# Kernel tuning notes

Measured on AMD Instinct MI355X. Metric: run time of the kernel, lower is better.

Reference implementation:

```python
import jax, jax.numpy as jnp
import numpy as np

N_SRC, N_TGT, N_EDGES = 100000, 50000, 1000000
S_IN, T_IN, S_OUT, T_OUT = 128, 128, 64, 64
NEG_SLOPE = 0.2


def setup_inputs() -> dict:
    key = jax.random.key(0)
    ks = jax.random.split(key, 7)
    return {
        "x_source": jax.random.normal(ks[0], (N_SRC, S_IN), jnp.float32),
        "x_target": jax.random.normal(ks[1], (N_TGT, T_IN), jnp.float32),
        "w_s": jax.random.normal(ks[2], (S_IN, T_OUT), jnp.float32) * 0.1,
        "w_t": jax.random.normal(ks[3], (T_IN, S_OUT), jnp.float32) * 0.1,
        "att_weight": jax.random.normal(ks[4], (T_OUT + S_OUT,), jnp.float32) * 0.1,
        "nbhd_values": jnp.ones((N_EDGES,), jnp.float32),
        "rows": jax.random.randint(ks[5], (N_EDGES,), 0, N_TGT, jnp.int32),  # target idx i
        "cols": jax.random.randint(ks[6], (N_EDGES,), 0, N_SRC, jnp.int32),  # source idx j
    }


def reference(x_source, x_target, w_s, w_t, att_weight, nbhd_values, rows, cols):
    n_src, n_tgt = x_source.shape[0], x_target.shape[0]
    t_out = w_s.shape[1]  # dim of s_message
    s_out = w_t.shape[1]  # dim of t_message

    s_msg = x_source @ w_s  # [n_src, t_out]
    t_msg = x_target @ w_t  # [n_tgt, s_out]

    # e_{ij} = LeakyReLU([s_msg_j || t_msg_i] . a); a = [a_s (t_out) || a_t (s_out)]
    a_s, a_t = att_weight[:t_out], att_weight[t_out:]
    # f uses permuted attention vector: [a[s_out:] || a[:s_out]] on [t_msg_j || s_msg_i]
    b_t, b_s = att_weight[s_out:], att_weight[:s_out]

    es = s_msg @ a_s  # [n_src]
    et = t_msg @ a_t  # [n_tgt]
    ft = t_msg @ b_t  # [n_tgt]
    fs = s_msg @ b_s  # [n_src]

    # s->t attention: rows are target cells (row-normalize over target rows)
    e = jax.nn.leaky_relu(es[cols] + et[rows], NEG_SLOPE)  # [E]
    e_den = jax.ops.segment_sum(e, rows, num_segments=n_tgt)
    att_st = e / e_den[rows]

    # t->s attention: transposed indices; rows are source cells
    f = jax.nn.leaky_relu(ft[rows] + fs[cols], NEG_SLOPE)  # [E]
    f_den = jax.ops.segment_sum(f, cols, num_segments=n_src)
    att_ts = f / f_den[cols]

    # Hadamard with neighborhood values, then sparse-dense aggregation
    w_st = att_st * nbhd_values  # [E]
    w_ts = att_ts * nbhd_values  # [E]

    message_on_target = jax.ops.segment_sum(w_st[:, None] * s_msg[cols], rows, num_segments=n_tgt)  # [n_tgt, t_out]
    message_on_source = jax.ops.segment_sum(w_ts[:, None] * t_msg[rows], cols, num_segments=n_src)  # [n_src, s_out]

    # update_func is None -> identity
    return message_on_source, message_on_target
```

## Files before the change

kernel.cpp:

```cpp
#include <hip/hip_runtime.h>

#define N_SRC   100000
#define N_TGT   50000
#define N_EDGES 1000000
#define NEG     0.2
#define NXCD    8
#define TPART   (N_TGT / NXCD)
#define SPART   (N_SRC / NXCD)

#define GBLK_S  1563
#define GBLK_T  782
#define GBLK    (GBLK_S + GBLK_T)
#define NHIST   640


#define XS2 65
__global__ __launch_bounds__(256) void fused_gemm_hist(
    const float* __restrict__ x_source, const float* __restrict__ x_target,
    const float* __restrict__ w_s, const float* __restrict__ w_t,
    const float* __restrict__ att,
    float* __restrict__ s_msg, float* __restrict__ t_msg,
    double* __restrict__ es_d, double* __restrict__ et_d,
    const int* __restrict__ rows, const int* __restrict__ cols,
    int* __restrict__ cnt_r, int* __restrict__ cnt_c,
    unsigned* __restrict__ packT, unsigned* __restrict__ packC)
{
    __shared__ float xs[64 * XS2];
    __shared__ double eds[4][64];
    const int tid = threadIdx.x;

    if (blockIdx.x < NHIST) {
        const int S = NHIST * 256;
        int i = blockIdx.x * 256 + tid;
        for (; i + 3 * S < N_EDGES; i += 4 * S) {
            const unsigned r0 = rows[i],         c0_ = cols[i];
            const unsigned r1 = rows[i + S],     c1_ = cols[i + S];
            const unsigned r2 = rows[i + 2 * S], c2_ = cols[i + 2 * S];
            const unsigned r3 = rows[i + 3 * S], c3_ = cols[i + 3 * S];
            const unsigned kr0 = atomicAdd(&cnt_r[r0], 1);
            const unsigned kc0 = atomicAdd(&cnt_c[c0_], 1);
            const unsigned kr1 = atomicAdd(&cnt_r[r1], 1);
            const unsigned kc1 = atomicAdd(&cnt_c[c1_], 1);
            const unsigned kr2 = atomicAdd(&cnt_r[r2], 1);
            const unsigned kc2 = atomicAdd(&cnt_c[c2_], 1);
            const unsigned kr3 = atomicAdd(&cnt_r[r3], 1);
            const unsigned kc3 = atomicAdd(&cnt_c[c3_], 1);
            packT[i]         = r0 | (kr0 << 16); packC[i]         = c0_ | (kc0 << 17);
            packT[i + S]     = r1 | (kr1 << 16); packC[i + S]     = c1_ | (kc1 << 17);
            packT[i + 2 * S] = r2 | (kr2 << 16); packC[i + 2 * S] = c2_ | (kc2 << 17);
            packT[i + 3 * S] = r3 | (kr3 << 16); packC[i + 3 * S] = c3_ | (kc3 << 17);
        }
        for (; i < N_EDGES; i += S) {
            const unsigned r = rows[i], c = cols[i];
            packT[i] = r | ((unsigned)atomicAdd(&cnt_r[r], 1) << 16);
            packC[i] = c | ((unsigned)atomicAdd(&cnt_c[c], 1) << 17);
        }
        return;
    }

    const int gi = blockIdx.x - NHIST;

    const float* x; const float* w; int att_off, nrows, bblk;
    float* msg; double* evec;
    if (gi < GBLK_S) { x = x_source; w = w_s; att_off = 0;  nrows = N_SRC;
                       msg = s_msg;  evec = es_d; bblk = gi; }
    else             { x = x_target; w = w_t; att_off = 64; nrows = N_TGT;
                       msg = t_msg;  evec = et_d; bblk = gi - GBLK_S; }

    const int lane = tid & 63;
    const int part = tid >> 6;
    const int c0   = __builtin_amdgcn_readfirstlane(part << 4);
    const int row0 = bblk * 64;
    const int row  = row0 + lane;
    const bool act = row < nrows;

    float acc[16];
    #pragma unroll
    for (int c = 0; c < 16; ++c) acc[c] = 0.f;

    const int xbase = lane * XS2;

    #pragma unroll
    for (int it = 0; it < 4; ++it) {
        const int fid = tid + it * 256;
        const int r = fid >> 4, q = fid & 15;
        if (row0 + r < nrows) {
            const float4 v = *(const float4*)(x + (size_t)(row0 + r) * 128 + 4 * q);
            float* d = &xs[r * XS2 + 4 * q];
            d[0] = v.x; d[1] = v.y; d[2] = v.z; d[3] = v.w;
        }
    }
    __syncthreads();

    float4 pre[4];
    #pragma unroll
    for (int it = 0; it < 4; ++it) {
        const int fid = tid + it * 256;
        const int r = fid >> 4, q = fid & 15;
        pre[it] = (row0 + r < nrows)
            ? *(const float4*)(x + (size_t)(row0 + r) * 128 + 64 + 4 * q)
            : make_float4(0.f, 0.f, 0.f, 0.f);
    }

    for (int kc = 0; kc < 64; kc += 16) {
        #pragma unroll
        for (int kk = 0; kk < 16; ++kk) {
            const float xk = xs[xbase + kc + kk];
            const float* wr = w + (size_t)(kc + kk) * 64 + c0;
            #pragma unroll
            for (int c = 0; c < 16; ++c)
                acc[c] = fmaf(xk, wr[c], acc[c]);
        }
    }
    __syncthreads();

    #pragma unroll
    for (int it = 0; it < 4; ++it) {
        const int fid = tid + it * 256;
        const int r = fid >> 4, q = fid & 15;
        float* d = &xs[r * XS2 + 4 * q];
        d[0] = pre[it].x; d[1] = pre[it].y; d[2] = pre[it].z; d[3] = pre[it].w;
    }
    __syncthreads();

    for (int kc = 0; kc < 64; kc += 16) {
        #pragma unroll
        for (int kk = 0; kk < 16; ++kk) {
            const float xk = xs[xbase + kc + kk];
            const float* wr = w + (size_t)(64 + kc + kk) * 64 + c0;
            #pragma unroll
            for (int c = 0; c < 16; ++c)
                acc[c] = fmaf(xk, wr[c], acc[c]);
        }
    }

    double e = 0.0;
    #pragma unroll
    for (int c = 0; c < 16; ++c)
        e += (double)acc[c] * (double)att[att_off + c0 + c];
    eds[part][lane] = e;
    __syncthreads();
    if (part == 0 && act)
        evec[row] = eds[0][lane] + eds[1][lane] + eds[2][lane] + eds[3][lane];

    if (act) {
        float* mo = msg + (size_t)row * 64 + c0;
        #pragma unroll
        for (int q = 0; q < 4; ++q)
            *(float4*)(mo + 4 * q) = *(float4*)(acc + 4 * q);
    }
}

__global__ __launch_bounds__(1024) void scan_two(
    const int* __restrict__ cnt_r, const int* __restrict__ cnt_c,
    int* __restrict__ ptr_r, int* __restrict__ ptr_c)
{
    const int n    = blockIdx.x ? N_SRC : N_TGT;
    const int* cnt = blockIdx.x ? cnt_c : cnt_r;
    int* ptr       = blockIdx.x ? ptr_c : ptr_r;
    const int tid  = threadIdx.x;
    const int lane = tid & 63, wid = tid >> 6;

    __shared__ int wsum[16];
    __shared__ int s_carry;
    if (tid == 0) s_carry = 0;
    __syncthreads();

    for (int base = 0; base < n; base += 4096) {
        const int idx = base + tid * 4;
        int4 v = make_int4(0, 0, 0, 0);
        if (idx + 3 < n) {
            v = *(const int4*)(cnt + idx);
        } else if (idx < n) {
            v.x = cnt[idx];
            if (idx + 1 < n) v.y = cnt[idx + 1];
            if (idx + 2 < n) v.z = cnt[idx + 2];
        }
        const int s = v.x + v.y + v.z + v.w;

        int p = s;
        #pragma unroll
        for (int d = 1; d < 64; d <<= 1) {
            int t = __shfl_up(p, d);
            if (lane >= d) p += t;
        }
        if (lane == 63) wsum[wid] = p;
        __syncthreads();
        if (tid == 0) {
            int a = 0;
            #pragma unroll
            for (int i = 0; i < 16; ++i) { int t = wsum[i]; wsum[i] = a; a += t; }
        }
        __syncthreads();

        int run = s_carry + wsum[wid] + (p - s);
        if (idx     < n) ptr[idx]     = run; run += v.x;
        if (idx + 1 < n) ptr[idx + 1] = run; run += v.y;
        if (idx + 2 < n) ptr[idx + 2] = run; run += v.z;
        if (idx + 3 < n) ptr[idx + 3] = run; run += v.w;

        __syncthreads();
        if (tid == 1023) s_carry = run;
        __syncthreads();
    }
    if (tid == 0) ptr[n] = s_carry;
}

__global__ __launch_bounds__(256) void scatter_part(
    const unsigned* __restrict__ packT, const unsigned* __restrict__ packC,
    const float* __restrict__ nbhd,
    const int* __restrict__ ptr_r, const int* __restrict__ ptr_c,
    unsigned long long* __restrict__ srtT, unsigned long long* __restrict__ srtS)
{
    const int xcd  = blockIdx.x & (NXCD - 1);
    const int ibx  = blockIdx.x >> 3;
    const int step = (gridDim.x >> 3) * blockDim.x;
    const unsigned lo_r = xcd * TPART, lo_c = xcd * SPART;

    for (int i = ibx * blockDim.x + threadIdx.x; i < N_EDGES; i += step) {
        const unsigned pT = packT[i], pC = packC[i];
        const unsigned r = pT & 0xFFFFu,  kr = pT >> 16;
        const unsigned c = pC & 0x1FFFFu, kc = pC >> 17;
        const bool mr = (r - lo_r) < TPART;
        const bool mc = (c - lo_c) < SPART;
        if (!(mr | mc)) continue;
        const unsigned long long nb =
            (unsigned long long)(unsigned)__float_as_int(nbhd[i]) << 32;
        if (mr) srtT[ptr_r[r] + kr] = nb | c;
        if (mc) srtS[ptr_c[c] + kc] = nb | r;
    }
}

__global__ __launch_bounds__(256) void gather_both(
    const int2* __restrict__ srtT, const int* __restrict__ ptr_r,
    const float* __restrict__ s_msg, float* __restrict__ msg_tgt,
    const int2* __restrict__ srtS, const int* __restrict__ ptr_c,
    const float* __restrict__ t_msg, float* __restrict__ msg_src,
    const double* __restrict__ es_d, const double* __restrict__ et_d)
{
    const int gw   = (blockIdx.x * blockDim.x + threadIdx.x) >> 6;
    const int lane = threadIdx.x & 63;

    const int2* srt; const int* ptr; const float* min_; float* out;
    const double* other_d; double base; int row;
    if (gw < N_TGT) {
        srt = srtT; ptr = ptr_r; min_ = s_msg; out = msg_tgt;
        other_d = es_d; row = gw; base = et_d[row];
    } else {
        row = gw - N_TGT;
        if (row >= N_SRC) return;
        srt = srtS; ptr = ptr_c; min_ = t_msg; out = msg_src;
        other_d = et_d; base = es_d[row];
    }

    const int b = ptr[row], e = ptr[row + 1];
    double den = 0.0;
    float a0 = 0.f, a1 = 0.f, a2 = 0.f, a3 = 0.f;

    for (int j0 = b; j0 < e; j0 += 64) {
        const int m = e - j0;
        int oidx = 0; double v = 0.0; float wf = 0.f;
        if (lane < m) {
            const int2 pay = srt[j0 + lane];
            oidx = pay.x;
            const float nb = __int_as_float(pay.y);
            const double sv = base + other_d[oidx];
            v = (sv >= 0.0) ? sv : NEG * sv;
            wf = (float)(v * (double)nb);
        }
        den += v;

        const int cnt = m < 64 ? m : 64;
        int j = 0;
        for (; j + 7 < cnt; j += 8) {
            const int   c0_ = __shfl(oidx, j);     const float w0 = __shfl(wf, j);
            const int   c1_ = __shfl(oidx, j + 1); const float w1 = __shfl(wf, j + 1);
            const int   c2_ = __shfl(oidx, j + 2); const float w2 = __shfl(wf, j + 2);
            const int   c3_ = __shfl(oidx, j + 3); const float w3 = __shfl(wf, j + 3);
            const int   c4_ = __shfl(oidx, j + 4); const float w4 = __shfl(wf, j + 4);
            const int   c5_ = __shfl(oidx, j + 5); const float w5 = __shfl(wf, j + 5);
            const int   c6_ = __shfl(oidx, j + 6); const float w6 = __shfl(wf, j + 6);
            const int   c7_ = __shfl(oidx, j + 7); const float w7 = __shfl(wf, j + 7);
            const float m0 = min_[(size_t)c0_ * 64 + lane];
            const float m1 = min_[(size_t)c1_ * 64 + lane];
            const float m2 = min_[(size_t)c2_ * 64 + lane];
            const float m3 = min_[(size_t)c3_ * 64 + lane];
            const float m4 = min_[(size_t)c4_ * 64 + lane];
            const float m5 = min_[(size_t)c5_ * 64 + lane];
            const float m6 = min_[(size_t)c6_ * 64 + lane];
            const float m7 = min_[(size_t)c7_ * 64 + lane];
            a0 = fmaf(w0, m0, a0); a1 = fmaf(w1, m1, a1);
            a2 = fmaf(w2, m2, a2); a3 = fmaf(w3, m3, a3);
            a0 = fmaf(w4, m4, a0); a1 = fmaf(w5, m5, a1);
            a2 = fmaf(w6, m6, a2); a3 = fmaf(w7, m7, a3);
        }
        for (; j + 3 < cnt; j += 4) {
            const int   c0_ = __shfl(oidx, j);     const float w0 = __shfl(wf, j);
            const int   c1_ = __shfl(oidx, j + 1); const float w1 = __shfl(wf, j + 1);
            const int   c2_ = __shfl(oidx, j + 2); const float w2 = __shfl(wf, j + 2);
            const int   c3_ = __shfl(oidx, j + 3); const float w3 = __shfl(wf, j + 3);
            a0 = fmaf(w0, min_[(size_t)c0_ * 64 + lane], a0);
            a1 = fmaf(w1, min_[(size_t)c1_ * 64 + lane], a1);
            a2 = fmaf(w2, min_[(size_t)c2_ * 64 + lane], a2);
            a3 = fmaf(w3, min_[(size_t)c3_ * 64 + lane], a3);
        }
        for (; j < cnt; ++j) {
            const int   c = __shfl(oidx, j);
            const float w = __shfl(wf, j);
            a0 = fmaf(w, min_[(size_t)c * 64 + lane], a0);
        }
    }
    #pragma unroll
    for (int s = 32; s; s >>= 1) den += __shfl_xor(den, s);
    const double inv = (den != 0.0) ? 1.0 / den : 0.0;
    const double acc = (double)((a0 + a1) + (a2 + a3));
    out[(size_t)row * 64 + lane] = (float)(acc * inv);
}

extern "C" void kernel_launch(void* const* d_in, const int* in_sizes, int n_in,
                              void* d_out, int out_size, void* d_ws, size_t ws_size,
                              hipStream_t stream)
{
    const float* x_source = (const float*)d_in[0];
    const float* x_target = (const float*)d_in[1];
    const float* w_s      = (const float*)d_in[2];
    const float* w_t      = (const float*)d_in[3];
    const float* att      = (const float*)d_in[4];
    const float* nbhd     = (const float*)d_in[5];
    const int*   rows     = (const int*)d_in[6];
    const int*   cols     = (const int*)d_in[7];

    float* out     = (float*)d_out;
    float* msg_src = out;
    float* msg_tgt = out + (size_t)N_SRC * 64;

    char* ws = (char*)d_ws;
    float*    s_msg  = (float*)   (ws + 0);
    float*    t_msg  = (float*)   (ws + 25600000);
    double*   es_d   = (double*)  (ws + 38400000);
    double*   et_d   = (double*)  (ws + 39200000);
    int*      cnt_r  = (int*)     (ws + 39600000);
    int*      cnt_c  = (int*)     (ws + 39800000);
    int*      ptr_r  = (int*)     (ws + 40200000);
    int*      ptr_c  = (int*)     (ws + 40400004);
    unsigned* packT  = (unsigned*)(ws + 40800016);
    unsigned* packC  = (unsigned*)(ws + 44800016);
    unsigned long long* srtT = (unsigned long long*)(ws + 48800016);
    unsigned long long* srtS = (unsigned long long*)(ws + 56800016);

    hipMemsetAsync(ws + 39600000, 0, 600000, stream);

    fused_gemm_hist<<<NHIST + GBLK, 256, 0, stream>>>(
        x_source, x_target, w_s, w_t, att,
        s_msg, t_msg, es_d, et_d,
        rows, cols, cnt_r, cnt_c, packT, packC);

    scan_two<<<2, 1024, 0, stream>>>(cnt_r, cnt_c, ptr_r, ptr_c);
    scatter_part<<<2048, 256, 0, stream>>>(
        packT, packC, nbhd, ptr_r, ptr_c, srtT, srtS);

    gather_both<<<(N_TGT + N_SRC + 3) / 4, 256, 0, stream>>>(
        (const int2*)srtT, ptr_r, s_msg, msg_tgt,
        (const int2*)srtS, ptr_c, t_msg, msg_src, es_d, et_d);
}
```

Before: 279.9 us.

## Bucket edges into per-XCD queues during histogram so scatter reads only local edges

The histogram phase now splits edges by target and source partition (one per XCD). Each block counts its matches, reserves space with one atomic, then uses wave ballots to compact edges into per-partition queues that carry the packed index, the other endpoint and the nbhd value. The scatter kernel then reads only its own partition's queue instead of rescanning all packed edges eight times. The cost is a double pass over rows and cols in the histogram blocks and 16-byte queue entries. The queues are stored in the output buffer as temporary space, which is safe only if gather writes over all of it afterwards.

```diff
diff --git a/kernel.cpp b/kernel.cpp
--- a/kernel.cpp
+++ b/kernel.cpp
@@ -11,54 +11,99 @@
 #define GBLK_S  1563
 #define GBLK_T  782
 #define GBLK    (GBLK_S + GBLK_T)
-#define NHIST   640
+#define NHQ     2048
+#define NSC     2048
+#define QCAP    131072
 
 
 #define XS2 65
-__global__ __launch_bounds__(256) void fused_gemm_hist(
+__global__ __launch_bounds__(256) void fused_histq_gemm(
+    const int* __restrict__ rows, const int* __restrict__ cols,
+    const float* __restrict__ nbhd,
+    int* __restrict__ cnt_r, int* __restrict__ cnt_c,
+    int* __restrict__ qtails, uint4* __restrict__ qT, uint4* __restrict__ qS,
     const float* __restrict__ x_source, const float* __restrict__ x_target,
     const float* __restrict__ w_s, const float* __restrict__ w_t,
     const float* __restrict__ att,
     float* __restrict__ s_msg, float* __restrict__ t_msg,
-    double* __restrict__ es_d, double* __restrict__ et_d,
-    const int* __restrict__ rows, const int* __restrict__ cols,
-    int* __restrict__ cnt_r, int* __restrict__ cnt_c,
-    unsigned* __restrict__ packT, unsigned* __restrict__ packC)
+    double* __restrict__ es_d, double* __restrict__ et_d)
 {
     __shared__ float xs[64 * XS2];
     __shared__ double eds[4][64];
+    __shared__ int hsum[8];
+    __shared__ int sbase[2];
+    __shared__ int stail[2];
     const int tid = threadIdx.x;
 
-    if (blockIdx.x < NHIST) {
-        const int S = NHIST * 256;
-        int i = blockIdx.x * 256 + tid;
-        for (; i + 3 * S < N_EDGES; i += 4 * S) {
-            const unsigned r0 = rows[i],         c0_ = cols[i];
-            const unsigned r1 = rows[i + S],     c1_ = cols[i + S];
-            const unsigned r2 = rows[i + 2 * S], c2_ = cols[i + 2 * S];
-            const unsigned r3 = rows[i + 3 * S], c3_ = cols[i + 3 * S];
-            const unsigned kr0 = atomicAdd(&cnt_r[r0], 1);
-            const unsigned kc0 = atomicAdd(&cnt_c[c0_], 1);
-            const unsigned kr1 = atomicAdd(&cnt_r[r1], 1);
-            const unsigned kc1 = atomicAdd(&cnt_c[c1_], 1);
-            const unsigned kr2 = atomicAdd(&cnt_r[r2], 1);
-            const unsigned kc2 = atomicAdd(&cnt_c[c2_], 1);
-            const unsigned kr3 = atomicAdd(&cnt_r[r3], 1);
-            const unsigned kc3 = atomicAdd(&cnt_c[c3_], 1);
-            packT[i]         = r0 | (kr0 << 16); packC[i]         = c0_ | (kc0 << 17);
-            packT[i + S]     = r1 | (kr1 << 16); packC[i + S]     = c1_ | (kc1 << 17);
-            packT[i + 2 * S] = r2 | (kr2 << 16); packC[i + 2 * S] = c2_ | (kc2 << 17);
-            packT[i + 3 * S] = r3 | (kr3 << 16); packC[i + 3 * S] = c3_ | (kc3 << 17);
-        }
-        for (; i < N_EDGES; i += S) {
-            const unsigned r = rows[i], c = cols[i];
-            packT[i] = r | ((unsigned)atomicAdd(&cnt_r[r], 1) << 16);
-            packC[i] = c | ((unsigned)atomicAdd(&cnt_c[c], 1) << 17);
+    if (blockIdx.x < NHQ) {
+        const int k    = blockIdx.x & 7;
+        const int ibx  = blockIdx.x >> 3;
+        const int lane = tid & 63, wid = tid >> 6;
+        const unsigned lo_r = k * TPART, lo_c = k * SPART;
+        const int step = (NHQ >> 3) * 256;
+
+        int nT = 0, nS = 0;
+        for (int ib = ibx * 256; ib < N_EDGES; ib += step) {
+            const int i = ib + tid;
+            unsigned r = 0xFFFFFFFFu, c = 0xFFFFFFFFu;
+            if (i < N_EDGES) { r = rows[i]; c = cols[i]; }
+            nT += ((r - lo_r) < TPART);
+            nS += ((c - lo_c) < SPART);
+        }
+        #pragma unroll
+        for (int d = 32; d; d >>= 1) { nT += __shfl_xor(nT, d); nS += __shfl_xor(nS, d); }
+        if (lane == 0) { hsum[wid] = nT; hsum[4 + wid] = nS; }
+        __syncthreads();
+        if (tid == 0) {
+            const int tT = hsum[0] + hsum[1] + hsum[2] + hsum[3];
+            const int tS = hsum[4] + hsum[5] + hsum[6] + hsum[7];
+            sbase[0] = atomicAdd(&qtails[k * 16],       tT);
+            sbase[1] = atomicAdd(&qtails[(8 + k) * 16], tS);
+            stail[0] = 0; stail[1] = 0;
+        }
+        __syncthreads();
+        const int bT = sbase[0], bS = sbase[1];
+        uint4* qTk = qT + (size_t)k * QCAP;
+        uint4* qSk = qS + (size_t)k * QCAP;
+
+        for (int ib = ibx * 256; ib < N_EDGES; ib += step) {
+            const int i = ib + tid;
+            unsigned r = 0xFFFFFFFFu, c = 0xFFFFFFFFu;
+            if (i < N_EDGES) { r = rows[i]; c = cols[i]; }
+            const bool mr = (r - lo_r) < TPART;
+            const bool mc = (c - lo_c) < SPART;
+            unsigned nbu = 0;
+            if (mr | mc) nbu = (unsigned)__float_as_int(nbhd[i]);
+
+            const unsigned long long mT = __ballot(mr);
+            if (mT) {
+                const int ldr = __ffsll((unsigned long long)mT) - 1;
+                int wb;
+                if (lane == ldr) wb = atomicAdd(&stail[0], (int)__popcll(mT));
+                wb = __shfl(wb, ldr);
+                if (mr) {
+                    const unsigned kr = (unsigned)atomicAdd(&cnt_r[r], 1);
+                    const int pos = bT + wb + (int)__popcll(mT & ((1ull << lane) - 1));
+                    qTk[pos] = make_uint4(r | (kr << 16), c, nbu, 0u);
+                }
+            }
+            const unsigned long long mS = __ballot(mc);
+            if (mS) {
+                const int ldr = __ffsll((unsigned long long)mS) - 1;
+                int wb;
+                if (lane == ldr) wb = atomicAdd(&stail[1], (int)__popcll(mS));
+                wb = __shfl(wb, ldr);
+                if (mc) {
+                    const unsigned kc = (unsigned)atomicAdd(&cnt_c[c], 1);
+                    const int pos = bS + wb + (int)__popcll(mS & ((1ull << lane) - 1));
+                    qSk[pos] = make_uint4(c | (kc << 17), r, nbu, 0u);
+                }
+            }
         }
         return;
     }
 
-    const int gi = blockIdx.x - NHIST;
+    const int gi = blockIdx.x - NHQ;
 
     const float* x; const float* w; int att_off, nrows, bblk;
     float* msg; double* evec;
@@ -206,28 +251,29 @@
     if (tid == 0) ptr[n] = s_carry;
 }
 
-__global__ __launch_bounds__(256) void scatter_part(
-    const unsigned* __restrict__ packT, const unsigned* __restrict__ packC,
-    const float* __restrict__ nbhd,
+__global__ __launch_bounds__(256) void scatter_queue(
+    const uint4* __restrict__ qT, const uint4* __restrict__ qS,
+    const int* __restrict__ qtails,
     const int* __restrict__ ptr_r, const int* __restrict__ ptr_c,
     unsigned long long* __restrict__ srtT, unsigned long long* __restrict__ srtS)
 {
-    const int xcd  = blockIdx.x & (NXCD - 1);
-    const int ibx  = blockIdx.x >> 3;
-    const int step = (gridDim.x >> 3) * blockDim.x;
-    const unsigned lo_r = xcd * TPART, lo_c = xcd * SPART;
-
-    for (int i = ibx * blockDim.x + threadIdx.x; i < N_EDGES; i += step) {
-        const unsigned pT = packT[i], pC = packC[i];
-        const unsigned r = pT & 0xFFFFu,  kr = pT >> 16;
-        const unsigned c = pC & 0x1FFFFu, kc = pC >> 17;
-        const bool mr = (r - lo_r) < TPART;
-        const bool mc = (c - lo_c) < SPART;
-        if (!(mr | mc)) continue;
-        const unsigned long long nb =
-            (unsigned long long)(unsigned)__float_as_int(nbhd[i]) << 32;
-        if (mr) srtT[ptr_r[r] + kr] = nb | c;
-        if (mc) srtS[ptr_c[c] + kc] = nb | r;
+    const int k   = blockIdx.x & 7;
+    const int ibx = blockIdx.x >> 3;
+    const int step = (NSC >> 3) * 256;
+    const int nT = qtails[k * 16];
+    const int nS = qtails[(8 + k) * 16];
+    const uint4* qTk = qT + (size_t)k * QCAP;
+    const uint4* qSk = qS + (size_t)k * QCAP;
+
+    for (int j = ibx * 256 + threadIdx.x; j < nT; j += step) {
+        const uint4 e = qTk[j];
+        const unsigned r = e.x & 0xFFFFu, kr = e.x >> 16;
+        srtT[ptr_r[r] + kr] = ((unsigned long long)e.z << 32) | e.y;
+    }
+    for (int j = ibx * 256 + threadIdx.x; j < nS; j += step) {
+        const uint4 e = qSk[j];
+        const unsigned c = e.x & 0x1FFFFu, kc = e.x >> 17;
+        srtS[ptr_c[c] + kc] = ((unsigned long long)e.z << 32) | e.y;
     }
 }
 
@@ -334,30 +380,33 @@
     float* msg_src = out;
     float* msg_tgt = out + (size_t)N_SRC * 64;
 
+    uint4* qT = (uint4*)d_out;
+    uint4* qS = (uint4*)((char*)d_out + (size_t)QCAP * 8 * 16);
+
     char* ws = (char*)d_ws;
-    float*    s_msg  = (float*)   (ws + 0);
-    float*    t_msg  = (float*)   (ws + 25600000);
-    double*   es_d   = (double*)  (ws + 38400000);
-    double*   et_d   = (double*)  (ws + 39200000);
-    int*      cnt_r  = (int*)     (ws + 39600000);
-    int*      cnt_c  = (int*)     (ws + 39800000);
-    int*      ptr_r  = (int*)     (ws + 40200000);
-    int*      ptr_c  = (int*)     (ws + 40400004);
-    unsigned* packT  = (unsigned*)(ws + 40800016);
-    unsigned* packC  = (unsigned*)(ws + 44800016);
-    unsigned long long* srtT = (unsigned long long*)(ws + 48800016);
-    unsigned long long* srtS = (unsigned long long*)(ws + 56800016);
-
-    hipMemsetAsync(ws + 39600000, 0, 600000, stream);
-
-    fused_gemm_hist<<<NHIST + GBLK, 256, 0, stream>>>(
+    float*  s_msg  = (float*) (ws + 0);
+    float*  t_msg  = (float*) (ws + 25600000);
+    double* es_d   = (double*)(ws + 38400000);
+    double* et_d   = (double*)(ws + 39200000);
+    int*    cnt_r  = (int*)   (ws + 39600000);
+    int*    cnt_c  = (int*)   (ws + 39800000);
+    int*    qtails = (int*)   (ws + 40200000);
+    int*    ptr_r  = (int*)   (ws + 40201024);
+    int*    ptr_c  = (int*)   (ws + 40401028);
+    unsigned long long* srtT = (unsigned long long*)(ws + 40801032);
+    unsigned long long* srtS = (unsigned long long*)(ws + 48801032);
+
+    hipMemsetAsync(ws + 39600000, 0, 601024, stream);
+
+    fused_histq_gemm<<<NHQ + GBLK, 256, 0, stream>>>(
+        rows, cols, nbhd, cnt_r, cnt_c, qtails, qT, qS,
         x_source, x_target, w_s, w_t, att,
-        s_msg, t_msg, es_d, et_d,
-        rows, cols, cnt_r, cnt_c, packT, packC);
+        s_msg, t_msg, es_d, et_d);
 
     scan_two<<<2, 1024, 0, stream>>>(cnt_r, cnt_c, ptr_r, ptr_c);
-    scatter_part<<<2048, 256, 0, stream>>>(
-        packT, packC, nbhd, ptr_r, ptr_c, srtT, srtS);
+
+    scatter_queue<<<NSC, 256, 0, stream>>>(
+        qT, qS, qtails, ptr_r, ptr_c, srtT, srtS);
 
     gather_both<<<(N_TGT + N_SRC + 3) / 4, 256, 0, stream>>>(
         (const int2*)srtT, ptr_r, s_msg, msg_tgt,
```

Measured after the change: 289.6 us. 3.5% more time.
